# Kernel tuning notes

Measured on AMD Instinct MI355X. Metric: run time of the kernel, lower is better.

Reference implementation:

```python
import jax, jax.numpy as jnp
import numpy as np

DT = 0.01  # constructor dt
T = 8_388_608  # number of timesteps


def setup_inputs() -> dict:
    key = jax.random.key(0)
    k1, k2 = jax.random.split(key)
    initial_state = jax.random.normal(k1, (1, 2), dtype=jnp.float32)
    actions = jax.random.normal(k2, (T, 1), dtype=jnp.float32)
    mass = jnp.float32(5.0)            # nn.Parameter init
    friction_coeff = jnp.float32(0.5)  # nn.Parameter init
    return {
        "initial_state": initial_state,
        "actions": actions,
        "mass": mass,
        "friction_coeff": friction_coeff,
    }


def reference(initial_state, actions, mass, friction_coeff):
    # Euler integration of 1D kinematics, rolled out with lax.scan
    # state: [1, 2] = [position, velocity]; actions: [T, 1]
    m_safe = jnp.abs(mass) + 0.001

    def step(state, action):
        x, v = state[:, 0], state[:, 1]
        F_applied = action  # [1]
        F_net = F_applied - friction_coeff * v
        a = F_net / m_safe
        v_next = v + a * DT
        x_next = x + v_next * DT
        s = jnp.stack([x_next, v_next], axis=1)  # [1, 2]
        return s, s

    _, traj = jax.lax.scan(step, initial_state, actions[:, 0][:, None])
    # traj: [T, 1, 2]; concatenate initial state like torch.cat(states, dim=0)
    states = jnp.concatenate([initial_state[None], traj], axis=0)  # [T+1, 1, 2]
    return states.reshape(-1, 2)  # [(T+1), 2]
```

## Files before the change

### kernel.cpp

```cpp
#include <hip/hip_runtime.h>
#include <math.h>


#define TPB 256
#define SEG 32
#define STEPS_PER_BLOCK (TPB * SEG)
#define POISON64 0xAAAAAAAAAAAAAAAAull
#define SLOT 8

__device__ __forceinline__ double ipow_d(double a, int n) {
    double r = 1.0, b = a;
    while (n) { if (n & 1) r *= b; b *= b; n >>= 1; }
    return r;
}

__device__ __forceinline__ double cgeom(double alpha, double An, int n) {
    const double DTd = (double)0.01f;
    double den = 1.0 - alpha;
    if (fabs(den) < 1e-12) return DTd * (double)n;
    return DTd * alpha * (1.0 - An) / den;
}

union F2U { unsigned long long u; float2 f; };

__global__ __launch_bounds__(TPB) void k1_reduce(
        const float* __restrict__ act,
        const float* __restrict__ mp,
        const float* __restrict__ fp,
        float4* __restrict__ thrPre,
        float2* __restrict__ blkAgg)
{
    __shared__ double sA[TPB], sB[TPB], sC[TPB], sD[TPB];
    const int t = threadIdx.x;
    const int g = blockIdx.x * TPB + t;

    const float m_safe = fabsf(mp[0]) + 0.001f;
    const float fric   = fp[0];
    const float DTf    = 0.01f;
    const float beta   = DTf / m_safe;
    const float alpha  = 1.0f - fric * beta;

    const float4* ap = (const float4*)(act + (size_t)g * SEG);
    float v = 0.0f, x = 0.0f;
#pragma unroll
    for (int i = 0; i < SEG / 4; ++i) {
        float4 a = ap[i];
        v = fmaf(alpha, v, beta * a.x); x = fmaf(v, DTf, x);
        v = fmaf(alpha, v, beta * a.y); x = fmaf(v, DTf, x);
        v = fmaf(alpha, v, beta * a.z); x = fmaf(v, DTf, x);
        v = fmaf(alpha, v, beta * a.w); x = fmaf(v, DTf, x);
    }

    const double ad  = 1.0 - (double)fric * ((double)0.01f) / (double)m_safe;
    const double A32 = ipow_d(ad, SEG);
    const double C32 = cgeom(ad, A32, SEG);

    sA[t] = A32; sB[t] = (double)v; sC[t] = C32; sD[t] = (double)x;
    __syncthreads();

    for (int d = 1; d < TPB; d <<= 1) {
        double a1, b1, c1, d1, a2, b2, c2, d2;
        const bool p = (t >= d);
        if (p) {
            a1 = sA[t - d]; b1 = sB[t - d]; c1 = sC[t - d]; d1 = sD[t - d];
            a2 = sA[t];     b2 = sB[t];     c2 = sC[t];     d2 = sD[t];
        }
        __syncthreads();
        if (p) {
            sA[t] = a2 * a1;
            sB[t] = fma(a2, b1, b2);
            sC[t] = fma(c2, a1, c1);
            sD[t] = fma(c2, b1, d1 + d2);
        }
        __syncthreads();
    }

    float4 pre;
    if (t == 0) pre = make_float4(1.0f, 0.0f, 0.0f, 0.0f);
    else        pre = make_float4((float)sA[t - 1], (float)sB[t - 1],
                                  (float)sC[t - 1], (float)sD[t - 1]);
    thrPre[g] = pre;
    if (t == TPB - 1)
        blkAgg[blockIdx.x] = make_float2((float)sB[TPB - 1], (float)sD[TPB - 1]);
}

__global__ __launch_bounds__(TPB) void kB_scan_emit(
        const float* __restrict__ act,
        const float4* __restrict__ thrPre,
        const float2* __restrict__ blkAgg,
        unsigned long long* blkPreU,
        const float* __restrict__ init,
        const float* __restrict__ mp,
        const float* __restrict__ fp,
        float2* __restrict__ out2,
        int nThreads, int nBlocks)
{
    __shared__ float4 sOut[TPB * 16];
    __shared__ float2 sBP;
    const int t = threadIdx.x;
    const int b = blockIdx.x;
    const int g = b * TPB + t;

    const float m_safe = fabsf(mp[0]) + 0.001f;
    const float fric   = fp[0];
    const float DTf    = 0.01f;
    const float beta   = DTf / m_safe;
    const float alpha  = 1.0f - fric * beta;

    const float4* ap = (const float4*)(act + (size_t)g * SEG);
    float4 a0 = ap[0], a1 = ap[1], a2 = ap[2], a3 = ap[3];
    float4 a4 = ap[4], a5 = ap[5], a6 = ap[6], a7 = ap[7];
    const float4 pm = thrPre[g];

    if (b == 0) {
        double* sA = (double*)sOut;
        double* sB = sA + TPB;
        double* sC = sB + TPB;
        double* sD = sC + TPB;

        const double ad = 1.0 - (double)fric * ((double)0.01f) / (double)m_safe;
        const double Ab = ipow_d(ad, STEPS_PER_BLOCK);
        const double Cb = cgeom(ad, Ab, STEPS_PER_BLOCK);

        const int G = nBlocks / TPB;
        double eB[4], eD[4];
        double aA = 1.0, aB = 0.0, aC = 0.0, aD = 0.0;
        for (int i = 0; i < G; ++i) {
            float2 bd = blkAgg[G * t + i];
            eB[i] = (double)bd.x; eD[i] = (double)bd.y;
            double nA = Ab * aA;
            double nB = fma(Ab, aB, eB[i]);
            double nC = aC + Cb * aA;
            double nD = aD + Cb * aB + eD[i];
            aA = nA; aB = nB; aC = nC; aD = nD;
        }
        sA[t] = aA; sB[t] = aB; sC[t] = aC; sD[t] = aD;
        __syncthreads();

        for (int d = 1; d < TPB; d <<= 1) {
            double a1s, b1s, c1s, d1s, a2s, b2s, c2s, d2s;
            const bool p = (t >= d);
            if (p) {
                a1s = sA[t - d]; b1s = sB[t - d]; c1s = sC[t - d]; d1s = sD[t - d];
                a2s = sA[t];     b2s = sB[t];     c2s = sC[t];     d2s = sD[t];
            }
            __syncthreads();
            if (p) {
                sA[t] = a2s * a1s;
                sB[t] = fma(a2s, b1s, b2s);
                sC[t] = fma(c2s, a1s, c1s);
                sD[t] = fma(c2s, b1s, d1s + d2s);
            }
            __syncthreads();
        }

        double pA, pB, pC, pD;
        if (t == 0) { pA = 1.0; pB = 0.0; pC = 0.0; pD = 0.0; }
        else        { pA = sA[t - 1]; pB = sB[t - 1]; pC = sC[t - 1]; pD = sD[t - 1]; }

        const double v0 = (double)init[1];
        const double x0 = (double)init[0];
        for (int i = 0; i < G; ++i) {
            F2U u;
            u.f = make_float2((float)fma(pA, v0, pB),
                              (float)(x0 + pC * v0 + pD));
            atomicExch(&blkPreU[(size_t)(G * t + i) * SLOT], u.u);
            double nA = Ab * pA;
            double nB = fma(Ab, pB, eB[i]);
            double nC = pC + Cb * pA;
            double nD = pD + Cb * pB + eD[i];
            pA = nA; pB = nB; pC = nC; pD = nD;
        }
        __syncthreads();
        if (t == 0) sBP = make_float2((float)v0, (float)x0);
        __syncthreads();
    } else {
        if (t == 0) {
            F2U u;
            u.u = atomicCAS(&blkPreU[(size_t)b * SLOT], POISON64, POISON64);
            while (u.u == POISON64) {
                __builtin_amdgcn_s_sleep(8);
                u.u = atomicCAS(&blkPreU[(size_t)b * SLOT], POISON64, POISON64);
            }
            sBP = u.f;
        }
        __syncthreads();
    }

    const float2 bp = sBP;
    float v = fmaf(pm.x, bp.x, pm.y);
    float x = bp.y + pm.z * bp.x + pm.w;

    float4* so = &sOut[t * 16];
    const int sw = t & 15;

    float4 aa[8] = {a0, a1, a2, a3, a4, a5, a6, a7};
#pragma unroll
    for (int q = 0; q < SEG / 4; ++q) {
        float4 a = aa[q];
        float4 e0, e1;
        e0.x = x; e0.y = v;
        v = fmaf(alpha, v, beta * a.x); x = fmaf(v, DTf, x);
        e0.z = x; e0.w = v;
        v = fmaf(alpha, v, beta * a.y); x = fmaf(v, DTf, x);
        e1.x = x; e1.y = v;
        v = fmaf(alpha, v, beta * a.z); x = fmaf(v, DTf, x);
        e1.z = x; e1.w = v;
        v = fmaf(alpha, v, beta * a.w); x = fmaf(v, DTf, x);
        so[(2 * q) ^ sw]     = e0;
        so[(2 * q + 1) ^ sw] = e1;
    }
    if (g == nThreads - 1)
        out2[(size_t)nThreads * SEG] = make_float2(x, v);

    __syncthreads();

    float4* o4 = (float4*)out2 + (size_t)b * (STEPS_PER_BLOCK / 2);
#pragma unroll
    for (int it = 0; it < 16; ++it) {
        const int j = t + it * TPB;
        const int src = (j & ~15) | ((j & 15) ^ ((j >> 4) & 15));
        o4[j] = sOut[src];
    }
}

extern "C" void kernel_launch(void* const* d_in, const int* in_sizes, int n_in,
                              void* d_out, int out_size, void* d_ws, size_t ws_size,
                              hipStream_t stream) {
    const float* init    = (const float*)d_in[0];
    const float* actions = (const float*)d_in[1];
    const float* mass    = (const float*)d_in[2];
    const float* fric    = (const float*)d_in[3];

    const int T = in_sizes[1];
    const int nThreads = T / SEG;
    const int nBlocks  = T / STEPS_PER_BLOCK;

    float4* thrPre = (float4*)d_ws;
    float2* blkAgg = (float2*)((char*)d_ws + (size_t)nThreads * 16);
    unsigned long long* blkPreU = (unsigned long long*)(blkAgg + nBlocks);

    k1_reduce<<<nBlocks, TPB, 0, stream>>>(actions, mass, fric, thrPre, blkAgg);
    kB_scan_emit<<<nBlocks, TPB, 0, stream>>>(actions, thrPre, blkAgg, blkPreU,
                                              init, mass, fric,
                                              (float2*)d_out, nThreads, nBlocks);
}
```

Measured before the change: 115.8 us.

## Fuse reduce and emit kernels into single-pass scan with block 0 aggregating

```diff
diff --git a/kernel.cpp b/kernel.cpp
--- a/kernel.cpp
+++ b/kernel.cpp
@@ -3,10 +3,15 @@
 
 
 #define TPB 256
-#define SEG 32
-#define STEPS_PER_BLOCK (TPB * SEG)
+#define SEGT 16
+#define TILES 2
+#define TILE_STEPS (TPB * SEGT)
+#define BLOCK_STEPS (TILE_STEPS * TILES)
+#define GPT 4
 #define POISON64 0xAAAAAAAAAAAAAAAAull
 #define SLOT 8
+
+union F2U { unsigned long long u; float2 f; };
 
 __device__ __forceinline__ double ipow_d(double a, int n) {
     double r = 1.0, b = a;
@@ -21,18 +26,25 @@
     return DTd * alpha * (1.0 - An) / den;
 }
 
-union F2U { unsigned long long u; float2 f; };
-
-__global__ __launch_bounds__(TPB) void k1_reduce(
+__global__ __launch_bounds__(TPB, 4) void k_fused(
         const float* __restrict__ act,
+        unsigned long long* aggU,
+        unsigned long long* preU,
+        const float* __restrict__ init,
         const float* __restrict__ mp,
         const float* __restrict__ fp,
-        float4* __restrict__ thrPre,
-        float2* __restrict__ blkAgg)
+        float2* __restrict__ out2,
+        int nBlocks)
 {
-    __shared__ double sA[TPB], sB[TPB], sC[TPB], sD[TPB];
+    __shared__ float4 sOut[TPB * 8];
+    __shared__ float2 sBP;
+    double* sA = (double*)sOut;
+    double* sB = sA + TPB;
+    double* sC = sB + TPB;
+    double* sD = sC + TPB;
+
     const int t = threadIdx.x;
-    const int g = blockIdx.x * TPB + t;
+    const int b = blockIdx.x;
 
     const float m_safe = fabsf(mp[0]) + 0.001f;
     const float fric   = fp[0];
@@ -40,147 +52,135 @@
     const float beta   = DTf / m_safe;
     const float alpha  = 1.0f - fric * beta;
 
-    const float4* ap = (const float4*)(act + (size_t)g * SEG);
-    float v = 0.0f, x = 0.0f;
-#pragma unroll
-    for (int i = 0; i < SEG / 4; ++i) {
-        float4 a = ap[i];
-        v = fmaf(alpha, v, beta * a.x); x = fmaf(v, DTf, x);
-        v = fmaf(alpha, v, beta * a.y); x = fmaf(v, DTf, x);
-        v = fmaf(alpha, v, beta * a.z); x = fmaf(v, DTf, x);
-        v = fmaf(alpha, v, beta * a.w); x = fmaf(v, DTf, x);
-    }
-
     const double ad  = 1.0 - (double)fric * ((double)0.01f) / (double)m_safe;
-    const double A32 = ipow_d(ad, SEG);
-    const double C32 = cgeom(ad, A32, SEG);
-
-    sA[t] = A32; sB[t] = (double)v; sC[t] = C32; sD[t] = (double)x;
-    __syncthreads();
-
-    for (int d = 1; d < TPB; d <<= 1) {
-        double a1, b1, c1, d1, a2, b2, c2, d2;
-        const bool p = (t >= d);
-        if (p) {
-            a1 = sA[t - d]; b1 = sB[t - d]; c1 = sC[t - d]; d1 = sD[t - d];
-            a2 = sA[t];     b2 = sB[t];     c2 = sC[t];     d2 = sD[t];
-        }
-        __syncthreads();
-        if (p) {
-            sA[t] = a2 * a1;
-            sB[t] = fma(a2, b1, b2);
-            sC[t] = fma(c2, a1, c1);
-            sD[t] = fma(c2, b1, d1 + d2);
-        }
-        __syncthreads();
-    }
-
-    float4 pre;
-    if (t == 0) pre = make_float4(1.0f, 0.0f, 0.0f, 0.0f);
-    else        pre = make_float4((float)sA[t - 1], (float)sB[t - 1],
-                                  (float)sC[t - 1], (float)sD[t - 1]);
-    thrPre[g] = pre;
-    if (t == TPB - 1)
-        blkAgg[blockIdx.x] = make_float2((float)sB[TPB - 1], (float)sD[TPB - 1]);
-}
-
-__global__ __launch_bounds__(TPB) void kB_scan_emit(
-        const float* __restrict__ act,
-        const float4* __restrict__ thrPre,
-        const float2* __restrict__ blkAgg,
-        unsigned long long* blkPreU,
-        const float* __restrict__ init,
-        const float* __restrict__ mp,
-        const float* __restrict__ fp,
-        float2* __restrict__ out2,
-        int nThreads, int nBlocks)
-{
-    __shared__ float4 sOut[TPB * 16];
-    __shared__ float2 sBP;
-    const int t = threadIdx.x;
-    const int b = blockIdx.x;
-    const int g = b * TPB + t;
-
-    const float m_safe = fabsf(mp[0]) + 0.001f;
-    const float fric   = fp[0];
-    const float DTf    = 0.01f;
-    const float beta   = DTf / m_safe;
-    const float alpha  = 1.0f - fric * beta;
-
-    const float4* ap = (const float4*)(act + (size_t)g * SEG);
-    float4 a0 = ap[0], a1 = ap[1], a2 = ap[2], a3 = ap[3];
-    float4 a4 = ap[4], a5 = ap[5], a6 = ap[6], a7 = ap[7];
-    const float4 pm = thrPre[g];
+    const double A16 = ipow_d(ad, SEGT);
+    const double C16 = cgeom(ad, A16, SEGT);
+    const double A4k = ipow_d(ad, TILE_STEPS);
+    const double C4k = cgeom(ad, A4k, TILE_STEPS);
+    const double A8k = A4k * A4k;
+    const double C8k = C4k + C4k * A4k;
+
+    float4 actv[TILES][4];
+#pragma unroll
+    for (int k = 0; k < TILES; ++k) {
+        const float4* p = (const float4*)(act + (size_t)b * BLOCK_STEPS
+                                          + k * TILE_STEPS + t * SEGT);
+        actv[k][0] = p[0]; actv[k][1] = p[1]; actv[k][2] = p[2]; actv[k][3] = p[3];
+    }
+
+    float preA[TILES], preB[TILES], preC[TILES], preD[TILES];
+    double tB0 = 0.0, tD0 = 0.0, tB1 = 0.0, tD1 = 0.0;
+#pragma unroll
+    for (int k = 0; k < TILES; ++k) {
+        float v = 0.0f, x = 0.0f;
+#pragma unroll
+        for (int q = 0; q < 4; ++q) {
+            float4 a = actv[k][q];
+            v = fmaf(alpha, v, beta * a.x); x = fmaf(v, DTf, x);
+            v = fmaf(alpha, v, beta * a.y); x = fmaf(v, DTf, x);
+            v = fmaf(alpha, v, beta * a.z); x = fmaf(v, DTf, x);
+            v = fmaf(alpha, v, beta * a.w); x = fmaf(v, DTf, x);
+        }
+        if (k > 0) __syncthreads();
+        sA[t] = A16; sB[t] = (double)v; sC[t] = C16; sD[t] = (double)x;
+        __syncthreads();
+        for (int d = 1; d < TPB; d <<= 1) {
+            double a1, b1, c1, d1, a2, b2, c2, d2;
+            const bool p = (t >= d);
+            if (p) {
+                a1 = sA[t-d]; b1 = sB[t-d]; c1 = sC[t-d]; d1 = sD[t-d];
+                a2 = sA[t];   b2 = sB[t];   c2 = sC[t];   d2 = sD[t];
+            }
+            __syncthreads();
+            if (p) {
+                sA[t] = a2 * a1;
+                sB[t] = fma(a2, b1, b2);
+                sC[t] = fma(c2, a1, c1);
+                sD[t] = fma(c2, b1, d1 + d2);
+            }
+            __syncthreads();
+        }
+        if (t == 0) { preA[k] = 1.f; preB[k] = 0.f; preC[k] = 0.f; preD[k] = 0.f; }
+        else {
+            preA[k] = (float)sA[t-1]; preB[k] = (float)sB[t-1];
+            preC[k] = (float)sC[t-1]; preD[k] = (float)sD[t-1];
+        }
+        const double tb = sB[TPB-1], td = sD[TPB-1];
+        if (k == 0) { tB0 = tb; tD0 = td; } else { tB1 = tb; tD1 = td; }
+    }
+
+    const double bB = fma(A4k, tB0, tB1);
+    const double bD = tD0 + C4k * tB0 + tD1;
+    if (t == 0) {
+        F2U u; u.f = make_float2((float)bB, (float)bD);
+        atomicExch(&aggU[(size_t)b * SLOT], u.u);
+    }
 
     if (b == 0) {
-        double* sA = (double*)sOut;
-        double* sB = sA + TPB;
-        double* sC = sB + TPB;
-        double* sD = sC + TPB;
-
-        const double ad = 1.0 - (double)fric * ((double)0.01f) / (double)m_safe;
-        const double Ab = ipow_d(ad, STEPS_PER_BLOCK);
-        const double Cb = cgeom(ad, Ab, STEPS_PER_BLOCK);
-
-        const int G = nBlocks / TPB;
-        double eB[4], eD[4];
-        double aA = 1.0, aB = 0.0, aC = 0.0, aD = 0.0;
-        for (int i = 0; i < G; ++i) {
-            float2 bd = blkAgg[G * t + i];
-            eB[i] = (double)bd.x; eD[i] = (double)bd.y;
-            double nA = Ab * aA;
-            double nB = fma(Ab, aB, eB[i]);
-            double nC = aC + Cb * aA;
-            double nD = aD + Cb * aB + eD[i];
-            aA = nA; aB = nB; aC = nC; aD = nD;
-        }
-        sA[t] = aA; sB[t] = aB; sC[t] = aC; sD[t] = aD;
-        __syncthreads();
-
+        double eB[GPT], eD[GPT];
+        double cA = 1.0, cB = 0.0, cC = 0.0, cD = 0.0;
+#pragma unroll
+        for (int i = 0; i < GPT; ++i) {
+            const int blk = GPT * t + i;
+            F2U u;
+            u.u = atomicCAS(&aggU[(size_t)blk * SLOT], POISON64, POISON64);
+            while (u.u == POISON64) {
+                __builtin_amdgcn_s_sleep(2);
+                u.u = atomicCAS(&aggU[(size_t)blk * SLOT], POISON64, POISON64);
+            }
+            eB[i] = (double)u.f.x; eD[i] = (double)u.f.y;
+            double nA = A8k * cA;
+            double nB = fma(A8k, cB, eB[i]);
+            double nC = cC + C8k * cA;
+            double nD = cD + C8k * cB + eD[i];
+            cA = nA; cB = nB; cC = nC; cD = nD;
+        }
+        __syncthreads();
+        sA[t] = cA; sB[t] = cB; sC[t] = cC; sD[t] = cD;
+        __syncthreads();
         for (int d = 1; d < TPB; d <<= 1) {
-            double a1s, b1s, c1s, d1s, a2s, b2s, c2s, d2s;
+            double a1, b1, c1, d1, a2, b2, c2, d2;
             const bool p = (t >= d);
             if (p) {
-                a1s = sA[t - d]; b1s = sB[t - d]; c1s = sC[t - d]; d1s = sD[t - d];
-                a2s = sA[t];     b2s = sB[t];     c2s = sC[t];     d2s = sD[t];
-            }
-            __syncthreads();
-            if (p) {
-                sA[t] = a2s * a1s;
-                sB[t] = fma(a2s, b1s, b2s);
-                sC[t] = fma(c2s, a1s, c1s);
-                sD[t] = fma(c2s, b1s, d1s + d2s);
-            }
-            __syncthreads();
-        }
-
+                a1 = sA[t-d]; b1 = sB[t-d]; c1 = sC[t-d]; d1 = sD[t-d];
+                a2 = sA[t];   b2 = sB[t];   c2 = sC[t];   d2 = sD[t];
+            }
+            __syncthreads();
+            if (p) {
+                sA[t] = a2 * a1;
+                sB[t] = fma(a2, b1, b2);
+                sC[t] = fma(c2, a1, c1);
+                sD[t] = fma(c2, b1, d1 + d2);
+            }
+            __syncthreads();
+        }
         double pA, pB, pC, pD;
         if (t == 0) { pA = 1.0; pB = 0.0; pC = 0.0; pD = 0.0; }
-        else        { pA = sA[t - 1]; pB = sB[t - 1]; pC = sC[t - 1]; pD = sD[t - 1]; }
+        else        { pA = sA[t-1]; pB = sB[t-1]; pC = sC[t-1]; pD = sD[t-1]; }
 
         const double v0 = (double)init[1];
         const double x0 = (double)init[0];
-        for (int i = 0; i < G; ++i) {
+#pragma unroll
+        for (int i = 0; i < GPT; ++i) {
             F2U u;
             u.f = make_float2((float)fma(pA, v0, pB),
                               (float)(x0 + pC * v0 + pD));
-            atomicExch(&blkPreU[(size_t)(G * t + i) * SLOT], u.u);
-            double nA = Ab * pA;
-            double nB = fma(Ab, pB, eB[i]);
-            double nC = pC + Cb * pA;
-            double nD = pD + Cb * pB + eD[i];
+            atomicExch(&preU[(size_t)(GPT * t + i) * SLOT], u.u);
+            double nA = A8k * pA;
+            double nB = fma(A8k, pB, eB[i]);
+            double nC = pC + C8k * pA;
+            double nD = pD + C8k * pB + eD[i];
             pA = nA; pB = nB; pC = nC; pD = nD;
         }
-        __syncthreads();
         if (t == 0) sBP = make_float2((float)v0, (float)x0);
         __syncthreads();
     } else {
         if (t == 0) {
             F2U u;
-            u.u = atomicCAS(&blkPreU[(size_t)b * SLOT], POISON64, POISON64);
+            u.u = atomicCAS(&preU[(size_t)b * SLOT], POISON64, POISON64);
             while (u.u == POISON64) {
                 __builtin_amdgcn_s_sleep(8);
-                u.u = atomicCAS(&blkPreU[(size_t)b * SLOT], POISON64, POISON64);
+                u.u = atomicCAS(&preU[(size_t)b * SLOT], POISON64, POISON64);
             }
             sBP = u.f;
         }
@@ -188,39 +188,48 @@
     }
 
     const float2 bp = sBP;
-    float v = fmaf(pm.x, bp.x, pm.y);
-    float x = bp.y + pm.z * bp.x + pm.w;
-
-    float4* so = &sOut[t * 16];
-    const int sw = t & 15;
-
-    float4 aa[8] = {a0, a1, a2, a3, a4, a5, a6, a7};
-#pragma unroll
-    for (int q = 0; q < SEG / 4; ++q) {
-        float4 a = aa[q];
-        float4 e0, e1;
-        e0.x = x; e0.y = v;
-        v = fmaf(alpha, v, beta * a.x); x = fmaf(v, DTf, x);
-        e0.z = x; e0.w = v;
-        v = fmaf(alpha, v, beta * a.y); x = fmaf(v, DTf, x);
-        e1.x = x; e1.y = v;
-        v = fmaf(alpha, v, beta * a.z); x = fmaf(v, DTf, x);
-        e1.z = x; e1.w = v;
-        v = fmaf(alpha, v, beta * a.w); x = fmaf(v, DTf, x);
-        so[(2 * q) ^ sw]     = e0;
-        so[(2 * q + 1) ^ sw] = e1;
-    }
-    if (g == nThreads - 1)
-        out2[(size_t)nThreads * SEG] = make_float2(x, v);
-
-    __syncthreads();
-
-    float4* o4 = (float4*)out2 + (size_t)b * (STEPS_PER_BLOCK / 2);
-#pragma unroll
-    for (int it = 0; it < 16; ++it) {
-        const int j = t + it * TPB;
-        const int src = (j & ~15) | ((j & 15) ^ ((j >> 4) & 15));
-        o4[j] = sOut[src];
+    double vtile = (double)bp.x, xtile = (double)bp.y;
+
+#pragma unroll
+    for (int k = 0; k < TILES; ++k) {
+        const float vt = (float)vtile, xt = (float)xtile;
+        float v = fmaf(preA[k], vt, preB[k]);
+        float x = xt + preC[k] * vt + preD[k];
+
+        float4* so = &sOut[t * 8];
+        const int sw = t & 7;
+#pragma unroll
+        for (int q = 0; q < 4; ++q) {
+            float4 a = actv[k][q];
+            float4 e0, e1;
+            e0.x = x; e0.y = v;
+            v = fmaf(alpha, v, beta * a.x); x = fmaf(v, DTf, x);
+            e0.z = x; e0.w = v;
+            v = fmaf(alpha, v, beta * a.y); x = fmaf(v, DTf, x);
+            e1.x = x; e1.y = v;
+            v = fmaf(alpha, v, beta * a.z); x = fmaf(v, DTf, x);
+            e1.z = x; e1.w = v;
+            v = fmaf(alpha, v, beta * a.w); x = fmaf(v, DTf, x);
+            so[(2 * q)     ^ sw] = e0;
+            so[(2 * q + 1) ^ sw] = e1;
+        }
+        if (k == TILES - 1 && b == nBlocks - 1 && t == TPB - 1)
+            out2[(size_t)nBlocks * BLOCK_STEPS] = make_float2(x, v);
+
+        __syncthreads();
+        float4* o4 = (float4*)out2 + ((size_t)b * BLOCK_STEPS + k * TILE_STEPS) / 2;
+#pragma unroll
+        for (int it = 0; it < 8; ++it) {
+            const int j = t + it * TPB;
+            const int src = (j & ~7) | ((j & 7) ^ ((j >> 3) & 7));
+            o4[j] = sOut[src];
+        }
+        if (k + 1 < TILES) {
+            const double nv = fma(A4k, vtile, tB0);
+            const double nx = xtile + C4k * vtile + tD0;
+            vtile = nv; xtile = nx;
+            __syncthreads();
+        }
     }
 }
 
@@ -233,15 +242,11 @@
     const float* fric    = (const float*)d_in[3];
 
     const int T = in_sizes[1];
-    const int nThreads = T / SEG;
-    const int nBlocks  = T / STEPS_PER_BLOCK;
-
-    float4* thrPre = (float4*)d_ws;
-    float2* blkAgg = (float2*)((char*)d_ws + (size_t)nThreads * 16);
-    unsigned long long* blkPreU = (unsigned long long*)(blkAgg + nBlocks);
-
-    k1_reduce<<<nBlocks, TPB, 0, stream>>>(actions, mass, fric, thrPre, blkAgg);
-    kB_scan_emit<<<nBlocks, TPB, 0, stream>>>(actions, thrPre, blkAgg, blkPreU,
-                                              init, mass, fric,
-                                              (float2*)d_out, nThreads, nBlocks);
-}
+    const int nBlocks = T / BLOCK_STEPS;
+
+    unsigned long long* aggU = (unsigned long long*)d_ws;
+    unsigned long long* preU = aggU + (size_t)nBlocks * SLOT;
+
+    k_fused<<<nBlocks, TPB, 0, stream>>>(actions, aggU, preU, init, mass, fric,
+                                         (float2*)d_out, nBlocks);
+}
```

Result: faster. 111.0 us (-4.2%).
